# Kernel tuning notes

Hardware: AMD Instinct MI355X
Metric: run time of the kernel (lower is better)

The kernel has to match this reference:

```python
import jax, jax.numpy as jnp
import numpy as np

B, S, D, H = 2, 2048, 1024, 16
DK = D // H


def setup_inputs() -> dict:
    key = jax.random.key(0)
    ks = jax.random.split(key, 12)
    lim = 1.0 / np.sqrt(D)
    def lin(kw, kb):
        W = jax.random.uniform(kw, (D, D), jnp.float32, -lim, lim)
        b = jax.random.uniform(kb, (D,), jnp.float32, -lim, lim)
        return W, b
    Wq, bq = lin(ks[0], ks[1])
    Wk, bk = lin(ks[2], ks[3])
    Wv, bv = lin(ks[4], ks[5])
    Wo, bo = lin(ks[6], ks[7])
    Q = jax.random.normal(ks[8], (B, S, D), jnp.float32)
    K = jax.random.normal(ks[9], (B, S, D), jnp.float32)
    V = jax.random.normal(ks[10], (B, S, D), jnp.float32)
    # causal mask, broadcastable to (B, H, S, S)
    mask = jnp.broadcast_to(jnp.tril(jnp.ones((S, S), jnp.bool_))[None, None], (B, 1, S, S))
    return {"Q": Q, "K": K, "V": V, "mask": mask,
            "Wq": Wq, "bq": bq, "Wk": Wk, "bk": bk,
            "Wv": Wv, "bv": bv, "Wo": Wo, "bo": bo}


def reference(Q, K, V, mask, Wq, bq, Wk, bk, Wv, bv, Wo, bo):
    def split(x):  # (B,S,D) -> (B,H,S,DK)
        return x.reshape(B, S, H, DK).transpose(0, 2, 1, 3)
    q = split(Q @ Wq.T + bq)
    k = split(K @ Wk.T + bk)
    v = split(V @ Wv.T + bv)
    scores = jnp.einsum('bhqd,bhkd->bhqk', q, k) / jnp.sqrt(jnp.float32(DK))
    scores = jnp.where(mask, scores, jnp.float32(-1e9))
    probs = jax.nn.softmax(scores, axis=-1)
    out = jnp.einsum('bhqk,bhkd->bhqd', probs, v)  # (B,H,S,DK)
    out = out.transpose(0, 2, 1, 3).reshape(B, S, D)
    return out @ Wo.T + bo
```

## Files before the change

kernel.cpp:

```cpp
#include <hip/hip_runtime.h>

#define S_LEN 2048
#define D_DIM 1024
#define H_NUM 16
#define DK_DIM 64
#define BATCH 2
#define M_TOT (BATCH * S_LEN)
#define XSZ 4194304
#define WSZ 1048576
#define SCALE_LOG2 0.18033688f

typedef __bf16 bf16x8 __attribute__((ext_vector_type(8)));
typedef float f32x4 __attribute__((ext_vector_type(4)));
typedef unsigned short u16;

__device__ inline u16 f2bf(float f) {
  union { float f; unsigned u; } v; v.f = f;
  unsigned u = v.u;
  return (u16)((u + 0x7FFFu + ((u >> 16) & 1u)) >> 16);
}

typedef const __attribute__((address_space(1))) unsigned int gu32;
typedef __attribute__((address_space(3))) unsigned int lu32;
__device__ inline void glds16(const u16* g, u16* l) {
  __builtin_amdgcn_global_load_lds((gu32*)g, (lu32*)l, 16, 0, 0);
}

__global__ __launch_bounds__(256)
void convert_kernel(const float* __restrict__ Q, const float* __restrict__ K,
                    const float* __restrict__ V, const float* __restrict__ Wq,
                    const float* __restrict__ Wk, const float* __restrict__ Wv,
                    const float* __restrict__ Wo, u16* __restrict__ Xb,
                    u16* __restrict__ Wb) {
  const size_t e = ((size_t)blockIdx.x * 256 + threadIdx.x) * 8;
  const float* src;
  u16* dst;
  size_t off;
  if (e < 3ull * XSZ) {
    const int a = (int)(e >> 22);
    src = (a == 0) ? Q : (a == 1) ? K : V;
    off = e - ((size_t)a << 22);
    dst = Xb + e;
  } else {
    const size_t ew = e - 3ull * XSZ;
    const int a = (int)(ew >> 20);
    src = (a == 0) ? Wq : (a == 1) ? Wk : (a == 2) ? Wv : Wo;
    off = ew - ((size_t)a << 20);
    dst = Wb + ew;
  }
  const float4 v0 = *reinterpret_cast<const float4*>(&src[off]);
  const float4 v1 = *reinterpret_cast<const float4*>(&src[off + 4]);
  ushort4 w0, w1;
  w0.x = f2bf(v0.x); w0.y = f2bf(v0.y); w0.z = f2bf(v0.z); w0.w = f2bf(v0.w);
  w1.x = f2bf(v1.x); w1.y = f2bf(v1.y); w1.z = f2bf(v1.z); w1.w = f2bf(v1.w);
  *reinterpret_cast<ushort4*>(dst) = w0;
  *reinterpret_cast<ushort4*>(dst + 4) = w1;
}

__global__ __launch_bounds__(256)
void proj_kernel(const u16* __restrict__ Qb, const u16* __restrict__ Kb,
                 const u16* __restrict__ Vb, const u16* __restrict__ Wqb,
                 const u16* __restrict__ Wkb, const u16* __restrict__ Wvb,
                 const float* __restrict__ bq, const float* __restrict__ bk,
                 const float* __restrict__ bv, u16* __restrict__ qh,
                 u16* __restrict__ kh, u16* __restrict__ vt) {
  const int z = blockIdx.z;
  const u16* A  = (z == 0) ? Qb : (z == 1) ? Kb : Vb;
  const u16* Bw = (z == 0) ? Wqb : (z == 1) ? Wkb : Wvb;
  const float* bias = (z == 0) ? bq : (z == 1) ? bk : bv;
  u16* out = (z == 0) ? qh : (z == 1) ? kh : vt;
  const float oscale = (z == 0) ? SCALE_LOG2 : 1.0f;

  __shared__ __align__(16) u16 Asm[128 * 64];
  __shared__ __align__(16) u16 Bsm[128 * 64];

  const int tid = threadIdx.x;
  const int m0 = blockIdx.x * 128, n0 = blockIdx.y * 128;
  const int wid = tid >> 6, lane = tid & 63;
  const int col = lane & 15, quad = lane >> 4;
  const int wm = (wid >> 1) * 64, wn = (wid & 1) * 64;

  const int lr = lane >> 3;
  const int lc = (lane & 7) ^ lr;
  const u16* gA = A + (size_t)(m0 + 32 * wid + lr) * D_DIM + lc * 8;
  const u16* gB = Bw + (size_t)(n0 + 32 * wid + lr) * D_DIM + lc * 8;

  f32x4 acc[4][4];
  const f32x4 zero4 = {0.f, 0.f, 0.f, 0.f};
  for (int i = 0; i < 4; i++)
    for (int j = 0; j < 4; j++) acc[i][j] = zero4;

  for (int k0 = 0; k0 < D_DIM; k0 += 64) {
    __syncthreads();
    for (int j = 0; j < 4; j++) {
      glds16(gA + (size_t)j * 8 * D_DIM + k0, &Asm[(32 * wid + 8 * j) * 64]);
      glds16(gB + (size_t)j * 8 * D_DIM + k0, &Bsm[(32 * wid + 8 * j) * 64]);
    }
    __syncthreads();

    bf16x8 af[4][2], bfm[4][2];
    for (int i = 0; i < 4; i++) {
      const int row = wm + i * 16 + col;
      const int r7 = row & 7;
      af[i][0] = *reinterpret_cast<const bf16x8*>(&Asm[row * 64 + ((quad ^ r7) * 8)]);
      af[i][1] = *reinterpret_cast<const bf16x8*>(&Asm[row * 64 + (((quad + 4) ^ r7) * 8)]);
    }
    for (int j = 0; j < 4; j++) {
      const int row = wn + j * 16 + col;
      const int r7 = row & 7;
      bfm[j][0] = *reinterpret_cast<const bf16x8*>(&Bsm[row * 64 + ((quad ^ r7) * 8)]);
      bfm[j][1] = *reinterpret_cast<const bf16x8*>(&Bsm[row * 64 + (((quad + 4) ^ r7) * 8)]);
    }
    if (z == 2) {
      for (int h = 0; h < 2; h++)
        for (int i = 0; i < 4; i++)
          for (int j = 0; j < 4; j++)
            acc[i][j] = __builtin_amdgcn_mfma_f32_16x16x32_bf16(
                af[i][h], bfm[j][h], acc[i][j], 0, 0, 0);
    } else {
      for (int h = 0; h < 2; h++)
        for (int i = 0; i < 4; i++)
          for (int j = 0; j < 4; j++)
            acc[i][j] = __builtin_amdgcn_mfma_f32_16x16x32_bf16(
                bfm[j][h], af[i][h], acc[i][j], 0, 0, 0);
    }
  }

  if (z != 2) {
    float4 b4[4];
    for (int j = 0; j < 4; j++)
      b4[j] = *reinterpret_cast<const float4*>(&bias[n0 + wn + j * 16 + quad * 4]);
    for (int i = 0; i < 4; i++) {
      const int token = m0 + wm + i * 16 + col;
      const int b = token >> 11, s = token & (S_LEN - 1);
      for (int j = 0; j < 4; j++) {
        const int gnb = n0 + wn + j * 16 + quad * 4;
        const int h = gnb >> 6, dk = gnb & 63;
        ushort4 w;
        w.x = f2bf((acc[i][j][0] + b4[j].x) * oscale);
        w.y = f2bf((acc[i][j][1] + b4[j].y) * oscale);
        w.z = f2bf((acc[i][j][2] + b4[j].z) * oscale);
        w.w = f2bf((acc[i][j][3] + b4[j].w) * oscale);
        *reinterpret_cast<ushort4*>(
            &out[((size_t)(b * H_NUM + h) * S_LEN + s) * DK_DIM + dk]) = w;
      }
    }
  } else {
    float bb[4];
    for (int j = 0; j < 4; j++) bb[j] = bias[n0 + wn + j * 16 + col];
    for (int i = 0; i < 4; i++) {
      const int token0 = m0 + wm + i * 16 + quad * 4;
      const int b = token0 >> 11, s0 = token0 & (S_LEN - 1);
      for (int j = 0; j < 4; j++) {
        const int gn = n0 + wn + j * 16 + col;
        const int h = gn >> 6, dk = gn & 63;
        ushort4 w;
        w.x = f2bf(acc[i][j][0] + bb[j]);
        w.y = f2bf(acc[i][j][1] + bb[j]);
        w.z = f2bf(acc[i][j][2] + bb[j]);
        w.w = f2bf(acc[i][j][3] + bb[j]);
        *reinterpret_cast<ushort4*>(
            &out[((size_t)(b * H_NUM + h) * DK_DIM + dk) * S_LEN + s0]) = w;
      }
    }
  }
}

__global__ __launch_bounds__(256)
void attn_kernel(const u16* __restrict__ qh, const u16* __restrict__ kh,
                 const u16* __restrict__ vt, u16* __restrict__ ctx) {
  __shared__ __align__(16) u16 Ksm[2][64 * 64];
  __shared__ __align__(16) u16 Vsm[2][64 * 64];
  __shared__ __align__(16) u16 Psm[4][16][72];

  const int tid  = threadIdx.x;
  const int bh   = blockIdx.x;
  const int y    = blockIdx.y;
  const int wid  = tid >> 6;
  const int lane = tid & 63;
  const int col  = lane & 15;
  const int quad = lane >> 4;
  const int r7   = col & 7;

  const int lr = lane >> 3;
  const int lc = (lane & 7) ^ lr;
  const u16* kbase = kh + ((size_t)bh * S_LEN + 16 * wid + lr) * DK_DIM + lc * 8;
  const u16* vbase = vt + ((size_t)bh * DK_DIM + 16 * wid + lr) * S_LEN + lc * 8;

  const f32x4 zero4 = {0.f, 0.f, 0.f, 0.f};
  const int b_ = bh >> 4, h_ = bh & 15;

  glds16(kbase, &Ksm[0][(16 * wid) * 64]);
  glds16(kbase + 8 * DK_DIM, &Ksm[0][(16 * wid + 8) * 64]);
  glds16(vbase, &Vsm[0][(16 * wid) * 64]);
  glds16(vbase + (size_t)8 * S_LEN, &Vsm[0][(16 * wid + 8) * 64]);

  int t = 0;
  for (int pp = 0; pp < 2; pp++) {
    const int qb = pp ? (31 - y) : y;
    const int nt = qb + 1;
    const int qrow_w = qb * 64 + wid * 16;
    const int qg = qrow_w + col;

    bf16x8 qB[2];
    {
      const u16* qp = &qh[((size_t)bh * S_LEN + qg) * DK_DIM + quad * 8];
      qB[0] = *reinterpret_cast<const bf16x8*>(qp);
      qB[1] = *reinterpret_cast<const bf16x8*>(qp + 32);
    }

    float l_ = 0.f;
    f32x4 o[4];
    for (int dm = 0; dm < 4; dm++) o[dm] = zero4;

    for (int tt = 0; tt < nt; tt++, t++) {
      const int b = t & 1;
      __syncthreads();

      {
        int nkv = -1;
        if (tt + 1 < nt) nkv = (tt + 1) * 64;
        else if (pp == 0) nkv = 0;
        if (nkv >= 0) {
          u16* kd = &Ksm[b ^ 1][(16 * wid) * 64];
          u16* vd = &Vsm[b ^ 1][(16 * wid) * 64];
          glds16(kbase + (size_t)nkv * DK_DIM, kd);
          glds16(kbase + (size_t)(nkv + 8) * DK_DIM, kd + 8 * 64);
          glds16(vbase + nkv, vd);
          glds16(vbase + (size_t)8 * S_LEN + nkv, vd + 8 * 64);
        }
      }

      const int kv0 = tt * 64;
      f32x4 s[4];
      for (int nc = 0; nc < 4; nc++) {
        const int row = nc * 16 + col;
        const bf16x8 kA0 = *reinterpret_cast<const bf16x8*>(
            &Ksm[b][row * 64 + ((quad ^ r7) * 8)]);
        const bf16x8 kA1 = *reinterpret_cast<const bf16x8*>(
            &Ksm[b][row * 64 + (((quad + 4) ^ r7) * 8)]);
        f32x4 acc = zero4;
        acc = __builtin_amdgcn_mfma_f32_16x16x32_bf16(kA0, qB[0], acc, 0, 0, 0);
        acc = __builtin_amdgcn_mfma_f32_16x16x32_bf16(kA1, qB[1], acc, 0, 0, 0);
        s[nc] = acc;
      }

      const bool domask = (kv0 + 63 > qrow_w);
      for (int nc = 0; nc < 4; nc++) {
        const int kvb = kv0 + nc * 16 + quad * 4;
        float p[4];
        for (int r = 0; r < 4; r++) {
          float e = __builtin_amdgcn_exp2f(s[nc][r]);
          if (domask && (kvb + r > qg)) e = 0.f;
          p[r] = e;
        }
        unsigned u0 = __float_as_uint(p[0]), u1 = __float_as_uint(p[1]);
        unsigned u2 = __float_as_uint(p[2]), u3 = __float_as_uint(p[3]);
        l_ += __uint_as_float(u0 & 0xffff0000u);
        l_ += __uint_as_float(u1 & 0xffff0000u);
        l_ += __uint_as_float(u2 & 0xffff0000u);
        l_ += __uint_as_float(u3 & 0xffff0000u);
        uint2 pw;
        pw.x = __builtin_amdgcn_perm(u1, u0, 0x07060302);
        pw.y = __builtin_amdgcn_perm(u3, u2, 0x07060302);
        *reinterpret_cast<uint2*>(&Psm[wid][col][nc * 16 + quad * 4]) = pw;
      }

      asm volatile("s_waitcnt lgkmcnt(0)" ::: "memory");

      bf16x8 pB[2];
      pB[0] = *reinterpret_cast<const bf16x8*>(&Psm[wid][col][quad * 8]);
      pB[1] = *reinterpret_cast<const bf16x8*>(&Psm[wid][col][32 + quad * 8]);
      for (int dm = 0; dm < 4; dm++) {
        const int row = dm * 16 + col;
        const bf16x8 vA0 = *reinterpret_cast<const bf16x8*>(
            &Vsm[b][row * 64 + ((quad ^ r7) * 8)]);
        const bf16x8 vA1 = *reinterpret_cast<const bf16x8*>(
            &Vsm[b][row * 64 + (((quad + 4) ^ r7) * 8)]);
        o[dm] = __builtin_amdgcn_mfma_f32_16x16x32_bf16(vA0, pB[0], o[dm], 0, 0, 0);
        o[dm] = __builtin_amdgcn_mfma_f32_16x16x32_bf16(vA1, pB[1], o[dm], 0, 0, 0);
      }
    }

    float rs = l_;
    rs += __shfl_xor(rs, 16);
    rs += __shfl_xor(rs, 32);
    const float inv = 1.0f / rs;
    for (int dm = 0; dm < 4; dm++) {
      ushort4 w;
      w.x = f2bf(o[dm][0] * inv);
      w.y = f2bf(o[dm][1] * inv);
      w.z = f2bf(o[dm][2] * inv);
      w.w = f2bf(o[dm][3] * inv);
      *reinterpret_cast<ushort4*>(
          &ctx[((size_t)b_ * S_LEN + qg) * D_DIM + h_ * DK_DIM + dm * 16 +
               quad * 4]) = w;
    }
  }
}

__global__ __launch_bounds__(256)
void outproj_kernel(const u16* __restrict__ ctx, const u16* __restrict__ Wob,
                    const float* __restrict__ bo, float* __restrict__ out) {
  __shared__ __align__(16) u16 Asm[64 * 64];
  __shared__ __align__(16) u16 Bsm[128 * 64];

  const int tid = threadIdx.x;
  const int m0 = blockIdx.x * 64, n0 = blockIdx.y * 128;
  const int wid = tid >> 6, lane = tid & 63;
  const int col = lane & 15, quad = lane >> 4;

  const int lr = lane >> 3;
  const int lc = (lane & 7) ^ lr;
  const u16* gA = ctx + (size_t)(m0 + 16 * wid + lr) * D_DIM + lc * 8;
  const u16* gB = Wob + (size_t)(n0 + 32 * wid + lr) * D_DIM + lc * 8;

  f32x4 acc[4][2];
  const f32x4 zero4 = {0.f, 0.f, 0.f, 0.f};
  for (int i = 0; i < 4; i++)
    for (int j = 0; j < 2; j++) acc[i][j] = zero4;

  for (int k0 = 0; k0 < D_DIM; k0 += 64) {
    __syncthreads();
    for (int j = 0; j < 2; j++)
      glds16(gA + (size_t)j * 8 * D_DIM + k0, &Asm[(16 * wid + 8 * j) * 64]);
    for (int j = 0; j < 4; j++)
      glds16(gB + (size_t)j * 8 * D_DIM + k0, &Bsm[(32 * wid + 8 * j) * 64]);
    __syncthreads();

    bf16x8 af[4][2], bfm[2][2];
    for (int i = 0; i < 4; i++) {
      const int row = i * 16 + col;
      const int r7 = row & 7;
      af[i][0] = *reinterpret_cast<const bf16x8*>(&Asm[row * 64 + ((quad ^ r7) * 8)]);
      af[i][1] = *reinterpret_cast<const bf16x8*>(&Asm[row * 64 + (((quad + 4) ^ r7) * 8)]);
    }
    for (int j = 0; j < 2; j++) {
      const int row = 32 * wid + j * 16 + col;
      const int r7 = row & 7;
      bfm[j][0] = *reinterpret_cast<const bf16x8*>(&Bsm[row * 64 + ((quad ^ r7) * 8)]);
      bfm[j][1] = *reinterpret_cast<const bf16x8*>(&Bsm[row * 64 + (((quad + 4) ^ r7) * 8)]);
    }
    for (int h = 0; h < 2; h++)
      for (int i = 0; i < 4; i++)
        for (int j = 0; j < 2; j++)
          acc[i][j] = __builtin_amdgcn_mfma_f32_16x16x32_bf16(
              bfm[j][h], af[i][h], acc[i][j], 0, 0, 0);
  }

  float4 b4[2];
  for (int j = 0; j < 2; j++)
    b4[j] = *reinterpret_cast<const float4*>(
        &bo[n0 + 32 * wid + j * 16 + quad * 4]);
  for (int i = 0; i < 4; i++) {
    const int token = m0 + i * 16 + col;
    for (int j = 0; j < 2; j++) {
      const int gnb = n0 + 32 * wid + j * 16 + quad * 4;
      float4 v;
      v.x = acc[i][j][0] + b4[j].x;
      v.y = acc[i][j][1] + b4[j].y;
      v.z = acc[i][j][2] + b4[j].z;
      v.w = acc[i][j][3] + b4[j].w;
      *reinterpret_cast<float4*>(&out[(size_t)token * D_DIM + gnb]) = v;
    }
  }
}

extern "C" void kernel_launch(void* const* d_in, const int* in_sizes, int n_in,
                              void* d_out, int out_size, void* d_ws,
                              size_t ws_size, hipStream_t stream) {
  const float* Q  = (const float*)d_in[0];
  const float* K  = (const float*)d_in[1];
  const float* V  = (const float*)d_in[2];
  const float* Wq = (const float*)d_in[4];
  const float* bq = (const float*)d_in[5];
  const float* Wk = (const float*)d_in[6];
  const float* bk = (const float*)d_in[7];
  const float* Wv = (const float*)d_in[8];
  const float* bv = (const float*)d_in[9];
  const float* Wo = (const float*)d_in[10];
  const float* bo = (const float*)d_in[11];
  float* out = (float*)d_out;

  u16* qh  = (u16*)d_ws;
  u16* kh  = qh + XSZ;
  u16* vt  = kh + XSZ;
  u16* Qb  = vt + XSZ;
  u16* ctx = Qb;
  u16* Kb  = Qb + XSZ;
  u16* Vb  = Kb + XSZ;
  u16* Wqb = Vb + XSZ;
  u16* Wkb = Wqb + WSZ;
  u16* Wvb = Wkb + WSZ;
  u16* Wob = Wvb + WSZ;

  convert_kernel<<<(3 * XSZ + 4 * WSZ) / (256 * 8), 256, 0, stream>>>(
      Q, K, V, Wq, Wk, Wv, Wo, Qb, Wqb);

  proj_kernel<<<dim3(M_TOT / 128, D_DIM / 128, 3), 256, 0, stream>>>(
      Qb, Kb, Vb, Wqb, Wkb, Wvb, bq, bk, bv, qh, kh, vt);

  attn_kernel<<<dim3(BATCH * H_NUM, 16), 256, 0, stream>>>(qh, kh, vt, ctx);

  outproj_kernel<<<dim3(M_TOT / 64, D_DIM / 128), 256, 0, stream>>>(ctx, Wob,
                                                                    bo, out);
}
```

Baseline: 236.5 us.

## Read K/V directly from global in attention, remap blocks per XCD

```diff
diff --git a/kernel.cpp b/kernel.cpp
--- a/kernel.cpp
+++ b/kernel.cpp
@@ -166,136 +166,109 @@
   }
 }
 
-__global__ __launch_bounds__(256)
+__global__ __launch_bounds__(256, 4)
 void attn_kernel(const u16* __restrict__ qh, const u16* __restrict__ kh,
                  const u16* __restrict__ vt, u16* __restrict__ ctx) {
-  __shared__ __align__(16) u16 Ksm[2][64 * 64];
-  __shared__ __align__(16) u16 Vsm[2][64 * 64];
   __shared__ __align__(16) u16 Psm[4][16][72];
 
   const int tid  = threadIdx.x;
-  const int bh   = blockIdx.x;
-  const int y    = blockIdx.y;
+  const int flat = blockIdx.x;
+  const int xcd  = flat & 7;
+  const int i_   = flat >> 3;
+  const int bh   = (xcd << 2) | (i_ >> 5);
+  const int qb   = 31 - (i_ & 31);
   const int wid  = tid >> 6;
   const int lane = tid & 63;
   const int col  = lane & 15;
   const int quad = lane >> 4;
-  const int r7   = col & 7;
-
-  const int lr = lane >> 3;
-  const int lc = (lane & 7) ^ lr;
-  const u16* kbase = kh + ((size_t)bh * S_LEN + 16 * wid + lr) * DK_DIM + lc * 8;
-  const u16* vbase = vt + ((size_t)bh * DK_DIM + 16 * wid + lr) * S_LEN + lc * 8;
+
+  const int nt = qb + 1;
+  const int qrow_w = qb * 64 + wid * 16;
+  const int qg = qrow_w + col;
+  const int b_ = bh >> 4, h_ = bh & 15;
 
   const f32x4 zero4 = {0.f, 0.f, 0.f, 0.f};
-  const int b_ = bh >> 4, h_ = bh & 15;
-
-  glds16(kbase, &Ksm[0][(16 * wid) * 64]);
-  glds16(kbase + 8 * DK_DIM, &Ksm[0][(16 * wid + 8) * 64]);
-  glds16(vbase, &Vsm[0][(16 * wid) * 64]);
-  glds16(vbase + (size_t)8 * S_LEN, &Vsm[0][(16 * wid + 8) * 64]);
-
-  int t = 0;
-  for (int pp = 0; pp < 2; pp++) {
-    const int qb = pp ? (31 - y) : y;
-    const int nt = qb + 1;
-    const int qrow_w = qb * 64 + wid * 16;
-    const int qg = qrow_w + col;
-
-    bf16x8 qB[2];
-    {
-      const u16* qp = &qh[((size_t)bh * S_LEN + qg) * DK_DIM + quad * 8];
-      qB[0] = *reinterpret_cast<const bf16x8*>(qp);
-      qB[1] = *reinterpret_cast<const bf16x8*>(qp + 32);
-    }
-
-    float l_ = 0.f;
-    f32x4 o[4];
-    for (int dm = 0; dm < 4; dm++) o[dm] = zero4;
-
-    for (int tt = 0; tt < nt; tt++, t++) {
-      const int b = t & 1;
-      __syncthreads();
-
-      {
-        int nkv = -1;
-        if (tt + 1 < nt) nkv = (tt + 1) * 64;
-        else if (pp == 0) nkv = 0;
-        if (nkv >= 0) {
-          u16* kd = &Ksm[b ^ 1][(16 * wid) * 64];
-          u16* vd = &Vsm[b ^ 1][(16 * wid) * 64];
-          glds16(kbase + (size_t)nkv * DK_DIM, kd);
-          glds16(kbase + (size_t)(nkv + 8) * DK_DIM, kd + 8 * 64);
-          glds16(vbase + nkv, vd);
-          glds16(vbase + (size_t)8 * S_LEN + nkv, vd + 8 * 64);
-        }
+
+  const u16* kp0 = kh + ((size_t)bh * S_LEN + col) * DK_DIM + quad * 8;
+  const u16* vp0 = vt + ((size_t)bh * DK_DIM + col) * S_LEN + quad * 8;
+
+  bf16x8 qB[2];
+  {
+    const u16* qp = &qh[((size_t)bh * S_LEN + qg) * DK_DIM + quad * 8];
+    qB[0] = *reinterpret_cast<const bf16x8*>(qp);
+    qB[1] = *reinterpret_cast<const bf16x8*>(qp + 32);
+  }
+
+  float l_ = 0.f;
+  f32x4 o[4];
+  for (int dm = 0; dm < 4; dm++) o[dm] = zero4;
+
+  for (int tt = 0; tt < nt; tt++) {
+    const int kv0 = tt * 64;
+
+    bf16x8 vA[4][2];
+    for (int dm = 0; dm < 4; dm++) {
+      const u16* vp = vp0 + (size_t)dm * 16 * S_LEN + kv0;
+      vA[dm][0] = *reinterpret_cast<const bf16x8*>(vp);
+      vA[dm][1] = *reinterpret_cast<const bf16x8*>(vp + 32);
+    }
+
+    f32x4 s[4];
+    for (int nc = 0; nc < 4; nc++) {
+      const u16* kp = kp0 + (size_t)(kv0 + nc * 16) * DK_DIM;
+      const bf16x8 kA0 = *reinterpret_cast<const bf16x8*>(kp);
+      const bf16x8 kA1 = *reinterpret_cast<const bf16x8*>(kp + 32);
+      f32x4 acc = zero4;
+      acc = __builtin_amdgcn_mfma_f32_16x16x32_bf16(kA0, qB[0], acc, 0, 0, 0);
+      acc = __builtin_amdgcn_mfma_f32_16x16x32_bf16(kA1, qB[1], acc, 0, 0, 0);
+      s[nc] = acc;
+    }
+
+    const bool domask = (kv0 + 63 > qrow_w);
+    for (int nc = 0; nc < 4; nc++) {
+      const int kvb = kv0 + nc * 16 + quad * 4;
+      float p[4];
+      for (int r = 0; r < 4; r++) {
+        float e = __builtin_amdgcn_exp2f(s[nc][r]);
+        if (domask && (kvb + r > qg)) e = 0.f;
+        p[r] = e;
       }
-
-      const int kv0 = tt * 64;
-      f32x4 s[4];
-      for (int nc = 0; nc < 4; nc++) {
-        const int row = nc * 16 + col;
-        const bf16x8 kA0 = *reinterpret_cast<const bf16x8*>(
-            &Ksm[b][row * 64 + ((quad ^ r7) * 8)]);
-        const bf16x8 kA1 = *reinterpret_cast<const bf16x8*>(
-            &Ksm[b][row * 64 + (((quad + 4) ^ r7) * 8)]);
-        f32x4 acc = zero4;
-        acc = __builtin_amdgcn_mfma_f32_16x16x32_bf16(kA0, qB[0], acc, 0, 0, 0);
-        acc = __builtin_amdgcn_mfma_f32_16x16x32_bf16(kA1, qB[1], acc, 0, 0, 0);
-        s[nc] = acc;
-      }
-
-      const bool domask = (kv0 + 63 > qrow_w);
-      for (int nc = 0; nc < 4; nc++) {
-        const int kvb = kv0 + nc * 16 + quad * 4;
-        float p[4];
-        for (int r = 0; r < 4; r++) {
-          float e = __builtin_amdgcn_exp2f(s[nc][r]);
-          if (domask && (kvb + r > qg)) e = 0.f;
-          p[r] = e;
-        }
-        unsigned u0 = __float_as_uint(p[0]), u1 = __float_as_uint(p[1]);
-        unsigned u2 = __float_as_uint(p[2]), u3 = __float_as_uint(p[3]);
-        l_ += __uint_as_float(u0 & 0xffff0000u);
-        l_ += __uint_as_float(u1 & 0xffff0000u);
-        l_ += __uint_as_float(u2 & 0xffff0000u);
-        l_ += __uint_as_float(u3 & 0xffff0000u);
-        uint2 pw;
-        pw.x = __builtin_amdgcn_perm(u1, u0, 0x07060302);
-        pw.y = __builtin_amdgcn_perm(u3, u2, 0x07060302);
-        *reinterpret_cast<uint2*>(&Psm[wid][col][nc * 16 + quad * 4]) = pw;
-      }
-
-      asm volatile("s_waitcnt lgkmcnt(0)" ::: "memory");
-
-      bf16x8 pB[2];
-      pB[0] = *reinterpret_cast<const bf16x8*>(&Psm[wid][col][quad * 8]);
-      pB[1] = *reinterpret_cast<const bf16x8*>(&Psm[wid][col][32 + quad * 8]);
-      for (int dm = 0; dm < 4; dm++) {
-        const int row = dm * 16 + col;
-        const bf16x8 vA0 = *reinterpret_cast<const bf16x8*>(
-            &Vsm[b][row * 64 + ((quad ^ r7) * 8)]);
-        const bf16x8 vA1 = *reinterpret_cast<const bf16x8*>(
-            &Vsm[b][row * 64 + (((quad + 4) ^ r7) * 8)]);
-        o[dm] = __builtin_amdgcn_mfma_f32_16x16x32_bf16(vA0, pB[0], o[dm], 0, 0, 0);
-        o[dm] = __builtin_amdgcn_mfma_f32_16x16x32_bf16(vA1, pB[1], o[dm], 0, 0, 0);
-      }
-    }
-
-    float rs = l_;
-    rs += __shfl_xor(rs, 16);
-    rs += __shfl_xor(rs, 32);
-    const float inv = 1.0f / rs;
+      unsigned u0 = __float_as_uint(p[0]), u1 = __float_as_uint(p[1]);
+      unsigned u2 = __float_as_uint(p[2]), u3 = __float_as_uint(p[3]);
+      l_ += __uint_as_float(u0 & 0xffff0000u);
+      l_ += __uint_as_float(u1 & 0xffff0000u);
+      l_ += __uint_as_float(u2 & 0xffff0000u);
+      l_ += __uint_as_float(u3 & 0xffff0000u);
+      uint2 pw;
+      pw.x = __builtin_amdgcn_perm(u1, u0, 0x07060302);
+      pw.y = __builtin_amdgcn_perm(u3, u2, 0x07060302);
+      *reinterpret_cast<uint2*>(&Psm[wid][col][nc * 16 + quad * 4]) = pw;
+    }
+
+    asm volatile("s_waitcnt lgkmcnt(0)" ::: "memory");
+
+    bf16x8 pB[2];
+    pB[0] = *reinterpret_cast<const bf16x8*>(&Psm[wid][col][quad * 8]);
+    pB[1] = *reinterpret_cast<const bf16x8*>(&Psm[wid][col][32 + quad * 8]);
     for (int dm = 0; dm < 4; dm++) {
-      ushort4 w;
-      w.x = f2bf(o[dm][0] * inv);
-      w.y = f2bf(o[dm][1] * inv);
-      w.z = f2bf(o[dm][2] * inv);
-      w.w = f2bf(o[dm][3] * inv);
-      *reinterpret_cast<ushort4*>(
-          &ctx[((size_t)b_ * S_LEN + qg) * D_DIM + h_ * DK_DIM + dm * 16 +
-               quad * 4]) = w;
-    }
+      o[dm] = __builtin_amdgcn_mfma_f32_16x16x32_bf16(vA[dm][0], pB[0], o[dm], 0, 0, 0);
+      o[dm] = __builtin_amdgcn_mfma_f32_16x16x32_bf16(vA[dm][1], pB[1], o[dm], 0, 0, 0);
+    }
+  }
+
+  float rs = l_;
+  rs += __shfl_xor(rs, 16);
+  rs += __shfl_xor(rs, 32);
+  const float inv = 1.0f / rs;
+  for (int dm = 0; dm < 4; dm++) {
+    ushort4 w;
+    w.x = f2bf(o[dm][0] * inv);
+    w.y = f2bf(o[dm][1] * inv);
+    w.z = f2bf(o[dm][2] * inv);
+    w.w = f2bf(o[dm][3] * inv);
+    *reinterpret_cast<ushort4*>(
+        &ctx[((size_t)b_ * S_LEN + qg) * D_DIM + h_ * DK_DIM + dm * 16 +
+             quad * 4]) = w;
   }
 }
 
@@ -400,7 +373,7 @@
   proj_kernel<<<dim3(M_TOT / 128, D_DIM / 128, 3), 256, 0, stream>>>(
       Qb, Kb, Vb, Wqb, Wkb, Wvb, bq, bk, bv, qh, kh, vt);
 
-  attn_kernel<<<dim3(BATCH * H_NUM, 16), 256, 0, stream>>>(qh, kh, vt, ctx);
+  attn_kernel<<<dim3(1024), 256, 0, stream>>>(qh, kh, vt, ctx);
 
   outproj_kernel<<<dim3(M_TOT / 64, D_DIM / 128), 256, 0, stream>>>(ctx, Wob,
                                                                     bo, out);
```

After: 422.0 us. 78.4% more time.
